# Optimization experiments

Hardware: AMD Instinct MI355X
Metric: run time of the kernel (lower is better)

The kernel has to match this reference:

```python
import jax, jax.numpy as jnp
import numpy as np

N, D, H = 4096, 1024, 16
HD = D // H  # head_dim = 64


def setup_inputs() -> dict:
    key = jax.random.key(0)
    ks = jax.random.split(key, 9)
    w_scale = 1.0 / np.sqrt(D)
    x = jax.random.normal(ks[0], (N, D), dtype=jnp.float32)
    Wq = jax.random.normal(ks[1], (D, D), dtype=jnp.float32) * w_scale
    bq = jax.random.normal(ks[2], (D,), dtype=jnp.float32) * w_scale
    Wk = jax.random.normal(ks[3], (D, D), dtype=jnp.float32) * w_scale
    bk = jax.random.normal(ks[4], (D,), dtype=jnp.float32) * w_scale
    Wv = jax.random.normal(ks[5], (D, D), dtype=jnp.float32) * w_scale
    bv = jax.random.normal(ks[6], (D,), dtype=jnp.float32) * w_scale
    Wo = jax.random.normal(ks[7], (D, D), dtype=jnp.float32) * w_scale
    bo = jax.random.normal(ks[8], (D,), dtype=jnp.float32) * w_scale
    return {"x": x, "Wq": Wq, "bq": bq, "Wk": Wk, "bk": bk,
            "Wv": Wv, "bv": bv, "Wo": Wo, "bo": bo}


def reference(x, Wq, bq, Wk, bk, Wv, bv, Wo, bo):
    # eqx.nn.Linear applies y = W @ x + b per token; vmapped over tokens -> x @ W.T + b
    q = (x @ Wq.T + bq).reshape(N, H, HD).transpose(1, 0, 2)  # [H, N, hd]
    k = (x @ Wk.T + bk).reshape(N, H, HD).transpose(1, 0, 2)  # [H, N, hd]
    v = (x @ Wv.T + bv).reshape(N, H, HD).transpose(1, 0, 2)  # [H, N, hd]
    scale = 1.0 / np.sqrt(HD)
    scores = jnp.einsum('hnd,hmd->hnm', q * scale, k)         # [H, N, N]
    attn = jax.nn.softmax(scores, axis=-1)
    ctx = jnp.einsum('hnm,hmd->hnd', attn, v)                 # [H, N, hd]
    ctx = ctx.transpose(1, 0, 2).reshape(N, D)                # [N, D]
    return ctx @ Wo.T + bo
```

## Files before the change

kernel.cpp:

```cpp
#include <hip/hip_runtime.h>
#include <hip/hip_bf16.h>

typedef __attribute__((ext_vector_type(8))) short short8;
typedef __attribute__((ext_vector_type(4))) float f32x4;
typedef __attribute__((ext_vector_type(16))) float f32x16;

#define MFMA16(a, b, c) __builtin_amdgcn_mfma_f32_16x16x32_bf16(a, b, c, 0, 0, 0)
#define MFMA32(a, b, c) __builtin_amdgcn_mfma_f32_32x32x16_bf16(a, b, c, 0, 0, 0)

typedef __attribute__((address_space(1))) const unsigned int GU32;
typedef __attribute__((address_space(3))) unsigned int LU32;
#define GLOAD16(g, l) __builtin_amdgcn_global_load_lds((GU32*)(g), (LU32*)(l), 16, 0, 0)

__device__ __forceinline__ unsigned short f2bf(float f) {
    union { float f; unsigned u; } a; a.f = f;
    unsigned r = a.u + 0x7fffu + ((a.u >> 16) & 1u);
    return (unsigned short)(r >> 16);
}

__device__ __forceinline__ unsigned pk2(float a, float b) {
    unsigned r;
    asm("v_cvt_pk_bf16_f32 %0, %1, %2" : "=v"(r) : "v"(a), "v"(b));
    return r;
}

#define CTXP_STRIDE (17u * 1024u * 1024u / 4u)

__global__ void cvt_all_k(const float* __restrict__ x,
                          const float* __restrict__ wq, const float* __restrict__ wk,
                          const float* __restrict__ wv, const float* __restrict__ wo,
                          unsigned short* __restrict__ xb,
                          unsigned short* __restrict__ wqb, unsigned short* __restrict__ wkb,
                          unsigned short* __restrict__ wvb, unsigned short* __restrict__ wob) {
    const int X4 = 4096 * 1024 / 4;
    const int W4 = 1024 * 1024 / 4;
    int i = blockIdx.x * 256 + threadIdx.x;
    const float* s; unsigned short* d; int off;
    if (i < X4) { s = x; d = xb; off = i; }
    else {
        int j = i - X4, w = j >> 18; off = j & (W4 - 1);
        s = w == 0 ? wq : (w == 1 ? wk : (w == 2 ? wv : wo));
        d = w == 0 ? wqb : (w == 1 ? wkb : (w == 2 ? wvb : wob));
    }
    float4 v = reinterpret_cast<const float4*>(s)[off];
    ushort4 o;
    o.x = f2bf(v.x); o.y = f2bf(v.y); o.z = f2bf(v.z); o.w = f2bf(v.w);
    reinterpret_cast<ushort4*>(d)[off] = o;
}

template<int MODE>
__global__ __launch_bounds__(256) void gemm_bt_k(
    const unsigned short* __restrict__ A,
    const unsigned short* __restrict__ B0, const unsigned short* __restrict__ B1,
    const unsigned short* __restrict__ B2,
    const float* __restrict__ bias0, const float* __restrict__ bias1, const float* __restrict__ bias2,
    float s0, float s1, float s2,
    void* o0, void* o1, void* o2)
{
    int bx, by, z;
    if (MODE == 0) {
        const int lin = blockIdx.x;
        const int swz = (lin & 7) * 96 + (lin >> 3);
        z = swz >> 8;
        const int r = swz & 255;
        bx = r >> 3; by = r & 7;
    } else { bx = blockIdx.x; by = blockIdx.y; z = blockIdx.z; }

    const unsigned short* B = z == 0 ? B0 : (z == 1 ? B1 : B2);
    const float* bias       = z == 0 ? bias0 : (z == 1 ? bias1 : bias2);
    const float scl         = z == 0 ? s0 : (z == 1 ? s1 : s2);
    void* outp              = z == 0 ? o0 : (z == 1 ? o1 : o2);

    __shared__ unsigned short As[2][4096];
    __shared__ unsigned short Bs[2][4096];

    const int tid = threadIdx.x;
    const int wid = tid >> 6, lane = tid & 63;
    const int lr = lane & 15, g = lane >> 4;
    const int wr = wid >> 1, wc = wid & 1;
    const int row0 = bx * 128;
    const int col0 = by * 128;

    const int srow = tid >> 2;
    const int scol = (tid & 3) * 8;
    const unsigned short* aS0 = A + (row0 + srow) * 1024 + scol;
    const unsigned short* aS1 = aS0 + 64 * 1024;
    const unsigned short* bS0 = B + (col0 + srow) * 1024 + scol;
    const unsigned short* bS1 = bS0 + 64 * 1024;
    unsigned short* lA = &As[0][wid * 512];
    unsigned short* lB = &Bs[0][wid * 512];

#define GSTG(BUF, K0) do {                              \
        GLOAD16(aS0 + (K0), lA + (BUF) * 4096);         \
        GLOAD16(aS1 + (K0), lA + (BUF) * 4096 + 2048);  \
        GLOAD16(bS0 + (K0), lB + (BUF) * 4096);         \
        GLOAD16(bS1 + (K0), lB + (BUF) * 4096 + 2048);  \
    } while (0)

    f32x4 acc[4][4] = {};

    auto cmp = [&](const unsigned short* Ab, const unsigned short* Bb) {
        short8 af[4], bfr[4];
#pragma unroll
        for (int m = 0; m < 4; ++m)
            af[m] = *(const short8*)(Ab + (wr * 64 + m * 16 + lr) * 32 + g * 8);
#pragma unroll
        for (int n = 0; n < 4; ++n)
            bfr[n] = *(const short8*)(Bb + (wc * 64 + n * 16 + lr) * 32 + g * 8);
#pragma unroll
        for (int m = 0; m < 4; ++m)
#pragma unroll
            for (int n = 0; n < 4; ++n)
                acc[m][n] = MFMA16(af[m], bfr[n], acc[m][n]);
    };

    GSTG(0, 0);
    __syncthreads();
    for (int k0 = 0; k0 < 1024; k0 += 64) {
        if (k0 + 32 < 1024) GSTG(1, k0 + 32);
        cmp(As[0], Bs[0]);
        __syncthreads();
        if (k0 + 64 < 1024) GSTG(0, k0 + 64);
        cmp(As[1], Bs[1]);
        __syncthreads();
    }
#undef GSTG

    const bool vtrans = (MODE == 0) && (z == 2);
#pragma unroll
    for (int n = 0; n < 4; ++n) {
        const int col = col0 + wc * 64 + n * 16 + lr;
        const float bv = bias[col];
#pragma unroll
        for (int m = 0; m < 4; ++m) {
            if (vtrans) {
                const int base16 = row0 + wr * 64 + m * 16;
                const int gp = ((g & 1) << 1) | (g >> 1);
                float v0 = acc[m][n][0] + bv, v1 = acc[m][n][1] + bv;
                float v2 = acc[m][n][2] + bv, v3 = acc[m][n][3] + bv;
                uint2 o; o.x = pk2(v0, v1); o.y = pk2(v2, v3);
                *(uint2*)((unsigned short*)outp + col * 4096 + base16 + gp * 4) = o;
            } else {
#pragma unroll
                for (int r = 0; r < 4; ++r) {
                    const int row = row0 + wr * 64 + m * 16 + g * 4 + r;
                    const float v = (acc[m][n][r] + bv) * scl;
                    if (MODE == 1) ((float*)outp)[row * 1024 + col] = v;
                    else           ((unsigned short*)outp)[row * 1024 + col] = f2bf(v);
                }
            }
        }
    }
}

__global__ __launch_bounds__(256) void gemm_out64_k(
    const unsigned short* __restrict__ A, const unsigned short* __restrict__ B,
    const float* __restrict__ bias, float* __restrict__ outp)
{
    __shared__ unsigned short As[2][2048];
    __shared__ unsigned short Bs[2][4096];

    const int tid = threadIdx.x;
    const int wid = tid >> 6, lane = tid & 63;
    const int lr = lane & 15, g = lane >> 4;
    const int wr = wid >> 1, wc = wid & 1;
    const int row0 = blockIdx.x * 64;
    const int col0 = blockIdx.y * 128;

    const int srow = tid >> 2;
    const int scol = (tid & 3) * 8;
    const unsigned short* aS0 = A + (row0 + srow) * 1024 + scol;
    const unsigned short* bS0 = B + (col0 + srow) * 1024 + scol;
    const unsigned short* bS1 = bS0 + 64 * 1024;
    unsigned short* lA = &As[0][wid * 512];
    unsigned short* lB = &Bs[0][wid * 512];

#define GSTG(BUF, K0) do {                              \
        GLOAD16(aS0 + (K0), lA + (BUF) * 2048);         \
        GLOAD16(bS0 + (K0), lB + (BUF) * 4096);         \
        GLOAD16(bS1 + (K0), lB + (BUF) * 4096 + 2048);  \
    } while (0)

    f32x4 acc[2][4] = {};

    auto cmp = [&](const unsigned short* Ab, const unsigned short* Bb) {
        short8 af[2], bfr[4];
#pragma unroll
        for (int m = 0; m < 2; ++m)
            af[m] = *(const short8*)(Ab + (wr * 32 + m * 16 + lr) * 32 + g * 8);
#pragma unroll
        for (int n = 0; n < 4; ++n)
            bfr[n] = *(const short8*)(Bb + (wc * 64 + n * 16 + lr) * 32 + g * 8);
#pragma unroll
        for (int m = 0; m < 2; ++m)
#pragma unroll
            for (int n = 0; n < 4; ++n)
                acc[m][n] = MFMA16(af[m], bfr[n], acc[m][n]);
    };

    GSTG(0, 0);
    __syncthreads();
    for (int k0 = 0; k0 < 1024; k0 += 64) {
        if (k0 + 32 < 1024) GSTG(1, k0 + 32);
        cmp(As[0], Bs[0]);
        __syncthreads();
        if (k0 + 64 < 1024) GSTG(0, k0 + 64);
        cmp(As[1], Bs[1]);
        __syncthreads();
    }
#undef GSTG

#pragma unroll
    for (int n = 0; n < 4; ++n) {
        const int col = col0 + wc * 64 + n * 16 + lr;
        const float bv = bias[col];
#pragma unroll
        for (int m = 0; m < 2; ++m)
#pragma unroll
            for (int r = 0; r < 4; ++r) {
                const int row = row0 + wr * 32 + m * 16 + g * 4 + r;
                outp[(size_t)row * 1024 + col] = acc[m][n][r] + bv;
            }
    }
}

template<int SPLIT>
__global__ __launch_bounds__(256, 2) void attn_core_k(
    const unsigned short* __restrict__ Q, const unsigned short* __restrict__ K,
    const unsigned short* __restrict__ Vt, unsigned short* __restrict__ C,
    float* __restrict__ ctxp, float* __restrict__ Lb)
{
    __shared__ unsigned short Ks[2][4096];
    __shared__ unsigned short Vs[2][4096];

    int h, q0, kvz;
    if (SPLIT == 2) {
        const int lin = blockIdx.x;
        const int xcd = lin & 7, slot = lin >> 3;
        const int grp = xcd * 4 + (slot >> 4);
        h   = grp & 15;
        kvz = grp >> 4;
        q0  = (slot & 15) * 256;
    } else {
        h = blockIdx.y; kvz = 0; q0 = blockIdx.x * 256;
    }
    const int NKV = 4096 / SPLIT;
    const int kvbase = kvz * NKV;
    const int tid = threadIdx.x, w = tid >> 6, lane = tid & 63;
    const int l31 = lane & 31, hi = lane >> 5;
    const int swz = (l31 & 7) << 4;
    const int qbase = q0 + w * 64;

    const int sr = tid >> 3;
    const int sb = (tid & 7) * 16;
    const int sc = (sb ^ ((sr & 7) << 4)) >> 1;
    const unsigned short* gK0 = K  + (size_t)(kvbase + sr) * 1024 + h * 64 + sc;
    const unsigned short* gK1 = gK0 + 32 * 1024;
    const unsigned short* gV0 = Vt + (size_t)(h * 64 + sr) * 4096 + kvbase + sc;
    const unsigned short* gV1 = gV0 + 32 * 4096;
    unsigned short* kd = &Ks[0][w * 512];
    unsigned short* vd = &Vs[0][w * 512];

#define ASTAGE(BUF, KV) do {                                          \
        GLOAD16(gK0 + (size_t)(KV) * 1024, kd + (BUF) * 4096);        \
        GLOAD16(gK1 + (size_t)(KV) * 1024, kd + (BUF) * 4096 + 2048); \
        GLOAD16(gV0 + (KV),        vd + (BUF) * 4096);                \
        GLOAD16(gV1 + (KV),        vd + (BUF) * 4096 + 2048);         \
    } while (0)

    short8 qfA[4], qfB[4];
    {
        const unsigned short* qpA = Q + (size_t)(qbase + l31) * 1024 + h * 64 + hi * 8;
        const unsigned short* qpB = qpA + 32 * 1024;
#pragma unroll
        for (int c = 0; c < 4; ++c) {
            qfA[c] = *(const short8*)(qpA + c * 16);
            qfB[c] = *(const short8*)(qpB + c * 16);
        }
    }

    int koff[4];
#pragma unroll
    for (int c = 0; c < 4; ++c) koff[c] = ((c * 32 + hi * 16) ^ swz) >> 1;

    f32x16 accA0 = {}, accA1 = {}, accB0 = {}, accB1 = {};
    float lhA = 0.f, lhB = 0.f;

    auto smx = [&](f32x16& s0, f32x16& s1, float& lh, unsigned* pf) {
        float p[32];
#pragma unroll
        for (int i = 0; i < 16; ++i) {
            p[i]      = __builtin_amdgcn_exp2f(s0[i]);
            p[16 + i] = __builtin_amdgcn_exp2f(s1[i]);
        }
        float u0 = 0.f, u1 = 0.f, u2 = 0.f, u3 = 0.f;
#pragma unroll
        for (int i = 0; i < 8; ++i) {
            u0 += p[i]; u1 += p[8 + i]; u2 += p[16 + i]; u3 += p[24 + i];
        }
        lh += (u0 + u1) + (u2 + u3);
#pragma unroll
        for (int c = 0; c < 4; ++c)
#pragma unroll
            for (int u = 0; u < 4; ++u)
                pf[c * 4 + u] = pk2(p[c * 8 + u * 2], p[c * 8 + u * 2 + 1]);
    };

    auto tile = [&](const unsigned short* Kc, const unsigned short* Vc) {
        f32x16 sA0 = {}, sA1 = {}, sB0 = {}, sB1 = {};
        __builtin_amdgcn_s_setprio(1);
#pragma unroll
        for (int c = 0; c < 4; ++c) {
            const short8 k0 = *(const short8*)(Kc + l31 * 64 + koff[c]);
            const short8 k1 = *(const short8*)(Kc + 2048 + l31 * 64 + koff[c]);
            sA0 = MFMA32(k0, qfA[c], sA0);
            sA1 = MFMA32(k1, qfA[c], sA1);
            sB0 = MFMA32(k0, qfB[c], sB0);
            sB1 = MFMA32(k1, qfB[c], sB1);
        }
        __builtin_amdgcn_s_setprio(0);
        unsigned pfA[16], pfB[16];
        smx(sA0, sA1, lhA, pfA);
        smx(sB0, sB1, lhB, pfB);
        __builtin_amdgcn_s_setprio(1);
#pragma unroll
        for (int c = 0; c < 4; ++c) {
            const short8 v0 = *(const short8*)(Vc + l31 * 64 + koff[c]);
            const short8 v1 = *(const short8*)(Vc + 2048 + l31 * 64 + koff[c]);
            union { unsigned u[4]; short8 s; } pA, pB;
#pragma unroll
            for (int u = 0; u < 4; ++u) { pA.u[u] = pfA[c * 4 + u]; pB.u[u] = pfB[c * 4 + u]; }
            accA0 = MFMA32(v0, pA.s, accA0);
            accA1 = MFMA32(v1, pA.s, accA1);
            accB0 = MFMA32(v0, pB.s, accB0);
            accB1 = MFMA32(v1, pB.s, accB1);
        }
        __builtin_amdgcn_s_setprio(0);
    };

    ASTAGE(0, 0);
    __syncthreads();
    for (int kv = 0; kv < NKV; kv += 128) {
        if (kv + 64 < NKV) ASTAGE(1, kv + 64);
        tile(Ks[0], Vs[0]);
        __syncthreads();
        if (kv + 128 < NKV) ASTAGE(0, kv + 128);
        tile(Ks[1], Vs[1]);
        __syncthreads();
    }
#undef ASTAGE

    const float lA = lhA + __shfl_xor(lhA, 32);
    const float lB = lhB + __shfl_xor(lhB, 32);

    if (SPLIT == 1) {
        const float liA = 1.f / lA, liB = 1.f / lB;
        unsigned short* CpA = C + (size_t)(qbase + l31) * 1024 + h * 64;
        unsigned short* CpB = CpA + 32 * 1024;
#pragma unroll
        for (int dt = 0; dt < 2; ++dt)
#pragma unroll
            for (int rq = 0; rq < 4; ++rq) {
                const f32x16& aA = dt ? accA1 : accA0;
                const f32x16& aB = dt ? accB1 : accB0;
                uint2 oA, oB;
                oA.x = pk2(aA[rq * 4 + 0] * liA, aA[rq * 4 + 1] * liA);
                oA.y = pk2(aA[rq * 4 + 2] * liA, aA[rq * 4 + 3] * liA);
                oB.x = pk2(aB[rq * 4 + 0] * liB, aB[rq * 4 + 1] * liB);
                oB.y = pk2(aB[rq * 4 + 2] * liB, aB[rq * 4 + 3] * liB);
                *(uint2*)(CpA + dt * 32 + rq * 8 + hi * 4) = oA;
                *(uint2*)(CpB + dt * 32 + rq * 8 + hi * 4) = oB;
            }
    } else {
        float* OpA = ctxp + (size_t)kvz * CTXP_STRIDE + (size_t)(qbase + l31) * 1024 + h * 64;
        float* OpB = OpA + 32 * 1024;
#pragma unroll
        for (int dt = 0; dt < 2; ++dt)
#pragma unroll
            for (int rq = 0; rq < 4; ++rq) {
                const f32x16& aA = dt ? accA1 : accA0;
                const f32x16& aB = dt ? accB1 : accB0;
                *(float4*)(OpA + dt * 32 + rq * 8 + hi * 4) =
                    make_float4(aA[rq * 4 + 0], aA[rq * 4 + 1], aA[rq * 4 + 2], aA[rq * 4 + 3]);
                *(float4*)(OpB + dt * 32 + rq * 8 + hi * 4) =
                    make_float4(aB[rq * 4 + 0], aB[rq * 4 + 1], aB[rq * 4 + 2], aB[rq * 4 + 3]);
            }
        const int q = qbase + hi * 32 + l31;
        Lb[((size_t)kvz * 16 + h) * 4096 + q] = hi ? lB : lA;
    }
}

__global__ __launch_bounds__(256) void combine_k(
    const float* __restrict__ ctxp, const float* __restrict__ Lb,
    unsigned short* __restrict__ C)
{
    int idx = blockIdx.x * 256 + threadIdx.x;
    int q = idx >> 7, d0 = (idx & 127) * 8, h = d0 >> 6;
    float L = Lb[(size_t)h * 4096 + q] + Lb[(size_t)(16 + h) * 4096 + q];
    const float inv = 1.f / L;
    const float4* p0 = (const float4*)(ctxp + (size_t)q * 1024 + d0);
    const float4* p1 = (const float4*)(ctxp + CTXP_STRIDE + (size_t)q * 1024 + d0);
    float4 a0 = p0[0], a1 = p0[1], b0 = p1[0], b1 = p1[1];
    uint4 o;
    o.x = pk2((a0.x + b0.x) * inv, (a0.y + b0.y) * inv);
    o.y = pk2((a0.z + b0.z) * inv, (a0.w + b0.w) * inv);
    o.z = pk2((a1.x + b1.x) * inv, (a1.y + b1.y) * inv);
    o.w = pk2((a1.z + b1.z) * inv, (a1.w + b1.w) * inv);
    *(uint4*)(C + (size_t)q * 1024 + d0) = o;
}

extern "C" void kernel_launch(void* const* d_in, const int* in_sizes, int n_in,
                              void* d_out, int out_size, void* d_ws, size_t ws_size,
                              hipStream_t stream) {
    const float* x  = (const float*)d_in[0];
    const float* Wq = (const float*)d_in[1];
    const float* bq = (const float*)d_in[2];
    const float* Wk = (const float*)d_in[3];
    const float* bk = (const float*)d_in[4];
    const float* Wv = (const float*)d_in[5];
    const float* bv = (const float*)d_in[6];
    const float* Wo = (const float*)d_in[7];
    const float* bo = (const float*)d_in[8];
    float* out = (float*)d_out;

    const size_t MB = 1ull << 20;
    char* ws = (char*)d_ws;
    unsigned short* xb  = (unsigned short*)(ws);
    unsigned short* Wqb = (unsigned short*)(ws + 8 * MB);
    unsigned short* Wkb = (unsigned short*)(ws + 10 * MB);
    unsigned short* Wvb = (unsigned short*)(ws + 12 * MB);
    unsigned short* Wob = (unsigned short*)(ws + 14 * MB);
    unsigned short* Qb  = (unsigned short*)(ws + 16 * MB);
    unsigned short* Kb  = (unsigned short*)(ws + 24 * MB);
    unsigned short* Vtb = (unsigned short*)(ws + 32 * MB);
    unsigned short* Cb  = xb;
    float* ctxp = (float*)(ws + 40 * MB);
    float* Lb2  = (float*)(ws + 74 * MB);

    cvt_all_k<<<8192, 256, 0, stream>>>(x, Wq, Wk, Wv, Wo, xb, Wqb, Wkb, Wvb, Wob);

    const float qscale = 0.125f * 1.4426950408889634f;
    gemm_bt_k<0><<<dim3(768, 1, 1), 256, 0, stream>>>(xb, Wqb, Wkb, Wvb, bq, bk, bv,
                                                      qscale, 1.f, 1.f, Qb, Kb, Vtb);

    if (ws_size >= 76 * MB) {
        attn_core_k<2><<<dim3(512, 1, 1), 256, 0, stream>>>(Qb, Kb, Vtb, Cb, ctxp, Lb2);
        combine_k<<<2048, 256, 0, stream>>>(ctxp, Lb2, Cb);
        gemm_out64_k<<<dim3(64, 8), 256, 0, stream>>>(Cb, Wob, bo, out);
    } else {
        attn_core_k<1><<<dim3(16, 16, 1), 256, 0, stream>>>(Qb, Kb, Vtb, Cb, nullptr, nullptr);
        gemm_bt_k<1><<<dim3(32, 8, 1), 256, 0, stream>>>(Cb, Wob, Wob, Wob, bo, bo, bo,
                                                         1.f, 1.f, 1.f, out, out, out);
    }
}
```

Baseline: 150.8 us.

## Replace split-KV attention with single-pass 32-row-per-wave kernel, drop combine

The attention kernel no longer splits the KV range in two with fp32 partial outputs and a separate combine pass. Each wave now handles 32 query rows instead of 64 over the full KV length, and 512 blocks of 128 queries are mapped per head with an XCD-aware index. This removes the partial-context writes and reads plus the combine launch, in exchange for each K/V tile being reused by fewer query rows. The QKV GEMM also drops its XCD swizzle and uses a plain 3D grid.

```diff
diff --git a/kernel.cpp b/kernel.cpp
--- a/kernel.cpp
+++ b/kernel.cpp
@@ -23,8 +23,6 @@
     asm("v_cvt_pk_bf16_f32 %0, %1, %2" : "=v"(r) : "v"(a), "v"(b));
     return r;
 }
-
-#define CTXP_STRIDE (17u * 1024u * 1024u / 4u)
 
 __global__ void cvt_all_k(const float* __restrict__ x,
                           const float* __restrict__ wq, const float* __restrict__ wk,
@@ -48,27 +46,18 @@
     reinterpret_cast<ushort4*>(d)[off] = o;
 }
 
-template<int MODE>
 __global__ __launch_bounds__(256) void gemm_bt_k(
     const unsigned short* __restrict__ A,
     const unsigned short* __restrict__ B0, const unsigned short* __restrict__ B1,
     const unsigned short* __restrict__ B2,
     const float* __restrict__ bias0, const float* __restrict__ bias1, const float* __restrict__ bias2,
-    float s0, float s1, float s2,
+    float s0,
     void* o0, void* o1, void* o2)
 {
-    int bx, by, z;
-    if (MODE == 0) {
-        const int lin = blockIdx.x;
-        const int swz = (lin & 7) * 96 + (lin >> 3);
-        z = swz >> 8;
-        const int r = swz & 255;
-        bx = r >> 3; by = r & 7;
-    } else { bx = blockIdx.x; by = blockIdx.y; z = blockIdx.z; }
-
+    const int z = blockIdx.z;
     const unsigned short* B = z == 0 ? B0 : (z == 1 ? B1 : B2);
     const float* bias       = z == 0 ? bias0 : (z == 1 ? bias1 : bias2);
-    const float scl         = z == 0 ? s0 : (z == 1 ? s1 : s2);
+    const float scl         = z == 0 ? s0 : 1.f;
     void* outp              = z == 0 ? o0 : (z == 1 ? o1 : o2);
 
     __shared__ unsigned short As[2][4096];
@@ -78,8 +67,8 @@
     const int wid = tid >> 6, lane = tid & 63;
     const int lr = lane & 15, g = lane >> 4;
     const int wr = wid >> 1, wc = wid & 1;
-    const int row0 = bx * 128;
-    const int col0 = by * 128;
+    const int row0 = blockIdx.x * 128;
+    const int col0 = blockIdx.y * 128;
 
     const int srow = tid >> 2;
     const int scol = (tid & 3) * 8;
@@ -126,7 +115,7 @@
     }
 #undef GSTG
 
-    const bool vtrans = (MODE == 0) && (z == 2);
+    const bool vtrans = (z == 2);
 #pragma unroll
     for (int n = 0; n < 4; ++n) {
         const int col = col0 + wc * 64 + n * 16 + lr;
@@ -145,8 +134,7 @@
                 for (int r = 0; r < 4; ++r) {
                     const int row = row0 + wr * 64 + m * 16 + g * 4 + r;
                     const float v = (acc[m][n][r] + bv) * scl;
-                    if (MODE == 1) ((float*)outp)[row * 1024 + col] = v;
-                    else           ((unsigned short*)outp)[row * 1024 + col] = f2bf(v);
+                    ((unsigned short*)outp)[row * 1024 + col] = f2bf(v);
                 }
             }
         }
@@ -224,39 +212,29 @@
     }
 }
 
-template<int SPLIT>
-__global__ __launch_bounds__(256, 2) void attn_core_k(
+__global__ __launch_bounds__(256, 2) void attn_k(
     const unsigned short* __restrict__ Q, const unsigned short* __restrict__ K,
-    const unsigned short* __restrict__ Vt, unsigned short* __restrict__ C,
-    float* __restrict__ ctxp, float* __restrict__ Lb)
+    const unsigned short* __restrict__ Vt, unsigned short* __restrict__ C)
 {
     __shared__ unsigned short Ks[2][4096];
     __shared__ unsigned short Vs[2][4096];
 
-    int h, q0, kvz;
-    if (SPLIT == 2) {
-        const int lin = blockIdx.x;
-        const int xcd = lin & 7, slot = lin >> 3;
-        const int grp = xcd * 4 + (slot >> 4);
-        h   = grp & 15;
-        kvz = grp >> 4;
-        q0  = (slot & 15) * 256;
-    } else {
-        h = blockIdx.y; kvz = 0; q0 = blockIdx.x * 256;
-    }
-    const int NKV = 4096 / SPLIT;
-    const int kvbase = kvz * NKV;
+    const int lin = blockIdx.x;
+    const int xcd = lin & 7, slot = lin >> 3;
+    const int h  = xcd + 8 * (slot >> 5);
+    const int q0 = (slot & 31) * 128;
+
     const int tid = threadIdx.x, w = tid >> 6, lane = tid & 63;
     const int l31 = lane & 31, hi = lane >> 5;
     const int swz = (l31 & 7) << 4;
-    const int qbase = q0 + w * 64;
+    const int qbase = q0 + w * 32;
 
     const int sr = tid >> 3;
     const int sb = (tid & 7) * 16;
     const int sc = (sb ^ ((sr & 7) << 4)) >> 1;
-    const unsigned short* gK0 = K  + (size_t)(kvbase + sr) * 1024 + h * 64 + sc;
+    const unsigned short* gK0 = K  + (size_t)sr * 1024 + h * 64 + sc;
     const unsigned short* gK1 = gK0 + 32 * 1024;
-    const unsigned short* gV0 = Vt + (size_t)(h * 64 + sr) * 4096 + kvbase + sc;
+    const unsigned short* gV0 = Vt + (size_t)(h * 64 + sr) * 4096 + sc;
     const unsigned short* gV1 = gV0 + 32 * 4096;
     unsigned short* kd = &Ks[0][w * 512];
     unsigned short* vd = &Vs[0][w * 512];
@@ -268,25 +246,29 @@
         GLOAD16(gV1 + (KV),        vd + (BUF) * 4096 + 2048);         \
     } while (0)
 
-    short8 qfA[4], qfB[4];
+    short8 qf[4];
     {
-        const unsigned short* qpA = Q + (size_t)(qbase + l31) * 1024 + h * 64 + hi * 8;
-        const unsigned short* qpB = qpA + 32 * 1024;
+        const unsigned short* qp = Q + (size_t)(qbase + l31) * 1024 + h * 64 + hi * 8;
+#pragma unroll
+        for (int c = 0; c < 4; ++c) qf[c] = *(const short8*)(qp + c * 16);
+    }
+
+    int koff[4];
+#pragma unroll
+    for (int c = 0; c < 4; ++c) koff[c] = ((c * 32 + hi * 16) ^ swz) >> 1;
+
+    f32x16 acc0 = {}, acc1 = {};
+    float lh = 0.f;
+
+    auto tile = [&](const unsigned short* Kc, const unsigned short* Vc) {
+        f32x16 s0 = {}, s1 = {};
+        __builtin_amdgcn_s_setprio(1);
 #pragma unroll
         for (int c = 0; c < 4; ++c) {
-            qfA[c] = *(const short8*)(qpA + c * 16);
-            qfB[c] = *(const short8*)(qpB + c * 16);
-        }
-    }
-
-    int koff[4];
-#pragma unroll
-    for (int c = 0; c < 4; ++c) koff[c] = ((c * 32 + hi * 16) ^ swz) >> 1;
-
-    f32x16 accA0 = {}, accA1 = {}, accB0 = {}, accB1 = {};
-    float lhA = 0.f, lhB = 0.f;
-
-    auto smx = [&](f32x16& s0, f32x16& s1, float& lh, unsigned* pf) {
+            s0 = MFMA32(*(const short8*)(Kc + l31 * 64 + koff[c]),        qf[c], s0);
+            s1 = MFMA32(*(const short8*)(Kc + 2048 + l31 * 64 + koff[c]), qf[c], s1);
+        }
+        __builtin_amdgcn_s_setprio(0);
         float p[32];
 #pragma unroll
         for (int i = 0; i < 16; ++i) {
@@ -299,114 +281,50 @@
             u0 += p[i]; u1 += p[8 + i]; u2 += p[16 + i]; u3 += p[24 + i];
         }
         lh += (u0 + u1) + (u2 + u3);
+        unsigned pf[16];
 #pragma unroll
         for (int c = 0; c < 4; ++c)
 #pragma unroll
             for (int u = 0; u < 4; ++u)
                 pf[c * 4 + u] = pk2(p[c * 8 + u * 2], p[c * 8 + u * 2 + 1]);
-    };
-
-    auto tile = [&](const unsigned short* Kc, const unsigned short* Vc) {
-        f32x16 sA0 = {}, sA1 = {}, sB0 = {}, sB1 = {};
         __builtin_amdgcn_s_setprio(1);
 #pragma unroll
         for (int c = 0; c < 4; ++c) {
-            const short8 k0 = *(const short8*)(Kc + l31 * 64 + koff[c]);
-            const short8 k1 = *(const short8*)(Kc + 2048 + l31 * 64 + koff[c]);
-            sA0 = MFMA32(k0, qfA[c], sA0);
-            sA1 = MFMA32(k1, qfA[c], sA1);
-            sB0 = MFMA32(k0, qfB[c], sB0);
-            sB1 = MFMA32(k1, qfB[c], sB1);
-        }
-        __builtin_amdgcn_s_setprio(0);
-        unsigned pfA[16], pfB[16];
-        smx(sA0, sA1, lhA, pfA);
-        smx(sB0, sB1, lhB, pfB);
-        __builtin_amdgcn_s_setprio(1);
-#pragma unroll
-        for (int c = 0; c < 4; ++c) {
-            const short8 v0 = *(const short8*)(Vc + l31 * 64 + koff[c]);
-            const short8 v1 = *(const short8*)(Vc + 2048 + l31 * 64 + koff[c]);
-            union { unsigned u[4]; short8 s; } pA, pB;
-#pragma unroll
-            for (int u = 0; u < 4; ++u) { pA.u[u] = pfA[c * 4 + u]; pB.u[u] = pfB[c * 4 + u]; }
-            accA0 = MFMA32(v0, pA.s, accA0);
-            accA1 = MFMA32(v1, pA.s, accA1);
-            accB0 = MFMA32(v0, pB.s, accB0);
-            accB1 = MFMA32(v1, pB.s, accB1);
+            union { unsigned u[4]; short8 s; } pa;
+#pragma unroll
+            for (int u = 0; u < 4; ++u) pa.u[u] = pf[c * 4 + u];
+            acc0 = MFMA32(*(const short8*)(Vc + l31 * 64 + koff[c]),        pa.s, acc0);
+            acc1 = MFMA32(*(const short8*)(Vc + 2048 + l31 * 64 + koff[c]), pa.s, acc1);
         }
         __builtin_amdgcn_s_setprio(0);
     };
 
     ASTAGE(0, 0);
     __syncthreads();
-    for (int kv = 0; kv < NKV; kv += 128) {
-        if (kv + 64 < NKV) ASTAGE(1, kv + 64);
+    for (int kv = 0; kv < 4096; kv += 128) {
+        if (kv + 64 < 4096) ASTAGE(1, kv + 64);
         tile(Ks[0], Vs[0]);
         __syncthreads();
-        if (kv + 128 < NKV) ASTAGE(0, kv + 128);
+        if (kv + 128 < 4096) ASTAGE(0, kv + 128);
         tile(Ks[1], Vs[1]);
         __syncthreads();
     }
 #undef ASTAGE
 
-    const float lA = lhA + __shfl_xor(lhA, 32);
-    const float lB = lhB + __shfl_xor(lhB, 32);
-
-    if (SPLIT == 1) {
-        const float liA = 1.f / lA, liB = 1.f / lB;
-        unsigned short* CpA = C + (size_t)(qbase + l31) * 1024 + h * 64;
-        unsigned short* CpB = CpA + 32 * 1024;
-#pragma unroll
-        for (int dt = 0; dt < 2; ++dt)
-#pragma unroll
-            for (int rq = 0; rq < 4; ++rq) {
-                const f32x16& aA = dt ? accA1 : accA0;
-                const f32x16& aB = dt ? accB1 : accB0;
-                uint2 oA, oB;
-                oA.x = pk2(aA[rq * 4 + 0] * liA, aA[rq * 4 + 1] * liA);
-                oA.y = pk2(aA[rq * 4 + 2] * liA, aA[rq * 4 + 3] * liA);
-                oB.x = pk2(aB[rq * 4 + 0] * liB, aB[rq * 4 + 1] * liB);
-                oB.y = pk2(aB[rq * 4 + 2] * liB, aB[rq * 4 + 3] * liB);
-                *(uint2*)(CpA + dt * 32 + rq * 8 + hi * 4) = oA;
-                *(uint2*)(CpB + dt * 32 + rq * 8 + hi * 4) = oB;
-            }
-    } else {
-        float* OpA = ctxp + (size_t)kvz * CTXP_STRIDE + (size_t)(qbase + l31) * 1024 + h * 64;
-        float* OpB = OpA + 32 * 1024;
-#pragma unroll
-        for (int dt = 0; dt < 2; ++dt)
-#pragma unroll
-            for (int rq = 0; rq < 4; ++rq) {
-                const f32x16& aA = dt ? accA1 : accA0;
-                const f32x16& aB = dt ? accB1 : accB0;
-                *(float4*)(OpA + dt * 32 + rq * 8 + hi * 4) =
-                    make_float4(aA[rq * 4 + 0], aA[rq * 4 + 1], aA[rq * 4 + 2], aA[rq * 4 + 3]);
-                *(float4*)(OpB + dt * 32 + rq * 8 + hi * 4) =
-                    make_float4(aB[rq * 4 + 0], aB[rq * 4 + 1], aB[rq * 4 + 2], aB[rq * 4 + 3]);
-            }
-        const int q = qbase + hi * 32 + l31;
-        Lb[((size_t)kvz * 16 + h) * 4096 + q] = hi ? lB : lA;
-    }
-}
-
-__global__ __launch_bounds__(256) void combine_k(
-    const float* __restrict__ ctxp, const float* __restrict__ Lb,
-    unsigned short* __restrict__ C)
-{
-    int idx = blockIdx.x * 256 + threadIdx.x;
-    int q = idx >> 7, d0 = (idx & 127) * 8, h = d0 >> 6;
-    float L = Lb[(size_t)h * 4096 + q] + Lb[(size_t)(16 + h) * 4096 + q];
-    const float inv = 1.f / L;
-    const float4* p0 = (const float4*)(ctxp + (size_t)q * 1024 + d0);
-    const float4* p1 = (const float4*)(ctxp + CTXP_STRIDE + (size_t)q * 1024 + d0);
-    float4 a0 = p0[0], a1 = p0[1], b0 = p1[0], b1 = p1[1];
-    uint4 o;
-    o.x = pk2((a0.x + b0.x) * inv, (a0.y + b0.y) * inv);
-    o.y = pk2((a0.z + b0.z) * inv, (a0.w + b0.w) * inv);
-    o.z = pk2((a1.x + b1.x) * inv, (a1.y + b1.y) * inv);
-    o.w = pk2((a1.z + b1.z) * inv, (a1.w + b1.w) * inv);
-    *(uint4*)(C + (size_t)q * 1024 + d0) = o;
+    const float l = lh + __shfl_xor(lh, 32);
+    const float li = 1.f / l;
+
+    unsigned short* Cp = C + (size_t)(qbase + l31) * 1024 + h * 64;
+#pragma unroll
+    for (int dt = 0; dt < 2; ++dt)
+#pragma unroll
+        for (int rq = 0; rq < 4; ++rq) {
+            const f32x16& a = dt ? acc1 : acc0;
+            uint2 o;
+            o.x = pk2(a[rq * 4 + 0] * li, a[rq * 4 + 1] * li);
+            o.y = pk2(a[rq * 4 + 2] * li, a[rq * 4 + 3] * li);
+            *(uint2*)(Cp + dt * 32 + rq * 8 + hi * 4) = o;
+        }
 }
 
 extern "C" void kernel_launch(void* const* d_in, const int* in_sizes, int n_in,
@@ -434,22 +352,14 @@
     unsigned short* Kb  = (unsigned short*)(ws + 24 * MB);
     unsigned short* Vtb = (unsigned short*)(ws + 32 * MB);
     unsigned short* Cb  = xb;
-    float* ctxp = (float*)(ws + 40 * MB);
-    float* Lb2  = (float*)(ws + 74 * MB);
 
     cvt_all_k<<<8192, 256, 0, stream>>>(x, Wq, Wk, Wv, Wo, xb, Wqb, Wkb, Wvb, Wob);
 
     const float qscale = 0.125f * 1.4426950408889634f;
-    gemm_bt_k<0><<<dim3(768, 1, 1), 256, 0, stream>>>(xb, Wqb, Wkb, Wvb, bq, bk, bv,
-                                                      qscale, 1.f, 1.f, Qb, Kb, Vtb);
-
-    if (ws_size >= 76 * MB) {
-        attn_core_k<2><<<dim3(512, 1, 1), 256, 0, stream>>>(Qb, Kb, Vtb, Cb, ctxp, Lb2);
-        combine_k<<<2048, 256, 0, stream>>>(ctxp, Lb2, Cb);
-        gemm_out64_k<<<dim3(64, 8), 256, 0, stream>>>(Cb, Wob, bo, out);
-    } else {
-        attn_core_k<1><<<dim3(16, 16, 1), 256, 0, stream>>>(Qb, Kb, Vtb, Cb, nullptr, nullptr);
-        gemm_bt_k<1><<<dim3(32, 8, 1), 256, 0, stream>>>(Cb, Wob, Wob, Wob, bo, bo, bo,
-                                                         1.f, 1.f, 1.f, out, out, out);
-    }
-}
+    gemm_bt_k<<<dim3(32, 8, 3), 256, 0, stream>>>(xb, Wqb, Wkb, Wvb, bq, bk, bv,
+                                                  qscale, Qb, Kb, Vtb);
+
+    attn_k<<<dim3(512, 1, 1), 256, 0, stream>>>(Qb, Kb, Vtb, Cb);
+
+    gemm_out64_k<<<dim3(64, 8), 256, 0, stream>>>(Cb, Wob, bo, out);
+}
```

After: 147.9 us. About the same (-2.0%).
